# Kernel optimization log

Measured on AMD Instinct MI355X. Metric: run time of the kernel, lower is better.

## Reference

```python
import jax, jax.numpy as jnp
import numpy as np

NUM_HEADS = 8
HIDDEN = 8

def conv1x1(x, w):
    # x: [B,C,H,W], w: [O,C] -> [B,O,H,W]
    return jnp.einsum('oc,bchw->bohw', w, x)

def grid_sample_border(img, gx, gy):
    # Bilinear grid_sample, padding_mode='border', align_corners=True.
    # img: [B,C,H,W]; gx, gy: [B,H,W] normalized coords in [-1,1].
    B, C, H, W = img.shape
    ix = (gx + 1.0) * 0.5 * (W - 1)
    iy = (gy + 1.0) * 0.5 * (H - 1)
    x0f = jnp.floor(ix); y0f = jnp.floor(iy)
    wx = (ix - x0f)[..., None]; wy = (iy - y0f)[..., None]
    x0 = x0f.astype(jnp.int32); y0 = y0f.astype(jnp.int32)
    x0c = jnp.clip(x0, 0, W - 1); x1c = jnp.clip(x0 + 1, 0, W - 1)
    y0c = jnp.clip(y0, 0, H - 1); y1c = jnp.clip(y0 + 1, 0, H - 1)
    imt = jnp.transpose(img, (0, 2, 3, 1))  # [B,H,W,C]
    b = jnp.arange(B)[:, None, None]
    v00 = imt[b, y0c, x0c]; v01 = imt[b, y0c, x1c]
    v10 = imt[b, y1c, x0c]; v11 = imt[b, y1c, x1c]
    out = (v00 * (1 - wx) * (1 - wy) + v01 * wx * (1 - wy)
           + v10 * (1 - wx) * wy + v11 * wx * wy)
    return jnp.transpose(out, (0, 3, 1, 2))

def process_sub(cur, ref, Wq, Wk, Wv, Wver, Whor):
    B, C, H, W = cur.shape
    c = HIDDEN // NUM_HEADS  # per-head channel dim (=1)
    q = conv1x1(cur, Wq).reshape(B, NUM_HEADS, c, H, W)
    k = conv1x1(ref, Wk).reshape(B, NUM_HEADS, c, H, W)
    v = conv1x1(ref, Wv).reshape(B, NUM_HEADS, c, H, W)
    # vertical axial attention (each column w independent, attend over rows)
    a_ver = jax.nn.softmax(jnp.einsum('bkchw,bkclw->bkwhl', q, k), axis=-1)
    o_ver = jnp.einsum('bkwhl,bkclw->bkchw', a_ver, v).reshape(B, HIDDEN, H, W)
    o_ver = conv1x1(o_ver, Wver)[:, 0]  # [B,H,W]
    # horizontal axial attention (each row h independent, attend over cols)
    a_hor = jax.nn.softmax(jnp.einsum('bkchw,bkchl->bkhwl', q, k), axis=-1)
    o_hor = jnp.einsum('bkhwl,bkchl->bkchw', a_hor, v).reshape(B, HIDDEN, H, W)
    o_hor = conv1x1(o_hor, Whor)[:, 0]  # [B,H,W]
    # identity grid + flow
    ys = -1.0 + 2.0 * jnp.arange(H, dtype=cur.dtype) / max(float(H - 1), 1.0)
    xs = -1.0 + 2.0 * jnp.arange(W, dtype=cur.dtype) / max(float(W - 1), 1.0)
    gx = xs[None, None, :] + o_hor / ((W - 1.0) / 2.0)
    gy = ys[None, :, None] + o_ver / ((H - 1.0) / 2.0)
    return grid_sample_border(ref, gx, gy)

def _forward(cur_fea, ref_fea, Wq, Wk, Wv, Wver, Whor):
    B, C, H, W = cur_fea.shape
    def split(x):
        return jnp.stack([x[:, :, ::2, ::2], x[:, :, 1::2, 1::2],
                          x[:, :, ::2, 1::2], x[:, :, 1::2, ::2]], 0)
    cur_sub = split(cur_fea).reshape(4 * B, C, H // 2, W // 2)
    ref_sub = split(ref_fea).reshape(4 * B, C, H // 2, W // 2)
    warped = process_sub(cur_sub, ref_sub, Wq, Wk, Wv, Wver, Whor)
    ul, br, ur, bl = warped.reshape(4, B, C, H // 2, W // 2)
    out = jnp.zeros((B, C, H, W), dtype=jnp.float32)
    out = out.at[:, :, ::2, ::2].set(ul)
    out = out.at[:, :, ::2, 1::2].set(ur)
    out = out.at[:, :, 1::2, ::2].set(bl)
    out = out.at[:, :, 1::2, 1::2].set(br)
    return out

def setup_inputs() -> dict:
    key = jax.random.key(0)
    ks = jax.random.split(key, 7)
    B, C, H, W = 2, 64, 256, 256
    return {
        'cur_fea': jax.random.normal(ks[0], (B, C, H, W), jnp.float32),
        'ref_fea': jax.random.normal(ks[1], (B, C, H, W), jnp.float32),
        'Wq': jax.random.normal(ks[2], (HIDDEN, C), jnp.float32) * 0.05,
        'Wk': jax.random.normal(ks[3], (HIDDEN, C), jnp.float32) * 0.05,
        'Wv': jax.random.normal(ks[4], (HIDDEN, C), jnp.float32) * 0.05,
        'Wver': jax.random.normal(ks[5], (1, HIDDEN), jnp.float32) * 0.05,
        'Whor': jax.random.normal(ks[6], (1, HIDDEN), jnp.float32) * 0.05,
    }

def reference(cur_fea, ref_fea, Wq, Wk, Wv, Wver, Whor):
    return _forward(cur_fea, ref_fea, Wq, Wk, Wv, Wver, Whor)
```

## Files before the change

kernel.cpp:

```cpp
#include <hip/hip_runtime.h>


constexpr int PLANE = 16384;
constexpr float LOG2E = 1.4426950408889634f;

typedef float v2f __attribute__((ext_vector_type(2)));

static __device__ __forceinline__ v2f pk_mul(v2f a, v2f b) {
    v2f d;
    asm("v_pk_mul_f32 %0, %1, %2" : "=v"(d) : "v"(a), "v"(b));
    return d;
}
static __device__ __forceinline__ void pk_addi(v2f& d, v2f a) {
    asm("v_pk_add_f32 %0, %0, %1" : "+v"(d) : "v"(a));
}
static __device__ __forceinline__ void pk_fmai(v2f& d, v2f a, v2f b) {
    asm("v_pk_fma_f32 %0, %1, %2, %0" : "+v"(d) : "v"(a), "v"(b));
}

__global__ __launch_bounds__(64) void prep_w(
    const float* __restrict__ Wq, const float* __restrict__ Wk,
    const float* __restrict__ Wv, float* __restrict__ WTg)
{
    const int c = threadIdx.x;
#pragma unroll
    for (int j = 0; j < 8; ++j) {
        WTg[c * 24 + j]      = Wq[j * 64 + c];
        WTg[c * 24 + 8 + j]  = LOG2E * Wk[j * 64 + c];
        WTg[c * 24 + 16 + j] = Wv[j * 64 + c];
    }
}

__global__ __launch_bounds__(512) void qkv_kernel(
    const float* __restrict__ cur, const float* __restrict__ ref,
    const float* __restrict__ WTg,
    float* __restrict__ Q, float* __restrict__ K, float* __restrict__ V)
{
    __shared__ float red0[128 * 25];
    __shared__ float red1[128 * 25];
    const int tid = threadIdx.x;

    const int bi = blockIdx.x;
    const int b  = bi >> 9;
    const int Y  = (bi >> 1) & 255;
    const int Xh = bi & 1;
    const int cg = tid >> 7;
    const int xi = tid & 127;
    const int X  = Xh * 128 + xi;

    const size_t base_in = (size_t)b * 64 * 65536 + (size_t)Y * 256 + X;
    const float* curp = cur + base_in;
    const float* refp = ref + base_in;

    float q[8], k[8], v[8];
#pragma unroll
    for (int i = 0; i < 8; ++i) { q[i] = 0.f; k[i] = 0.f; v[i] = 0.f; }

    const int c0 = __builtin_amdgcn_readfirstlane(cg * 16);
#pragma unroll 8
    for (int c = 0; c < 16; ++c) {
        float cu = curp[(size_t)(c0 + c) * 65536];
        float rf = refp[(size_t)(c0 + c) * 65536];
        const float* wr = &WTg[(c0 + c) * 24];
#pragma unroll
        for (int i = 0; i < 8; ++i) {
            q[i] = fmaf(wr[i],      cu, q[i]);
            k[i] = fmaf(wr[8 + i],  rf, k[i]);
            v[i] = fmaf(wr[16 + i], rf, v[i]);
        }
    }

    float* row0 = &red0[xi * 25];
    float* row1 = &red1[xi * 25];
    if (cg == 1) {
#pragma unroll
        for (int i = 0; i < 8; ++i) {
            row0[i] = q[i]; row0[8 + i] = k[i]; row0[16 + i] = v[i];
        }
    } else if (cg == 3) {
#pragma unroll
        for (int i = 0; i < 8; ++i) {
            row1[i] = q[i]; row1[8 + i] = k[i]; row1[16 + i] = v[i];
        }
    }
    __syncthreads();
    if (cg == 2) {
#pragma unroll
        for (int i = 0; i < 8; ++i) {
            row1[i]      += q[i];
            row1[8 + i]  += k[i];
            row1[16 + i] += v[i];
        }
    } else if (cg == 0) {
#pragma unroll
        for (int i = 0; i < 8; ++i) {
            q[i] += row0[i]; k[i] += row0[8 + i]; v[i] += row0[16 + i];
        }
    }
    __syncthreads();
    if (cg == 0) {
        const int dy = Y & 1, dx = X & 1;
        const int p  = dy ? (dx ? 1 : 3) : (dx ? 2 : 0);
        const int sb = p * 2 + b;
        const int h = Y >> 1, w = X >> 1;
#pragma unroll
        for (int i = 0; i < 8; ++i) {
            const size_t o = ((size_t)(sb * 8 + i) << 14) + (h << 7) + w;
            Q[o] = q[i] + row1[i];
            K[o] = k[i] + row1[8 + i];
            V[o] = v[i] + row1[16 + i];
        }
    }
}

__global__ __launch_bounds__(256) void attn_fused(
    const float* __restrict__ Q, const float* __restrict__ K,
    const float* __restrict__ V,
    const float* __restrict__ Whor, const float* __restrict__ Wver,
    float* __restrict__ OH, float* __restrict__ OVT)
{
    __shared__ __align__(16) float kk[4][2 * 132];
    __shared__ __align__(16) float vv[4][2 * 132];
    __shared__ float part[4 * 128];

    const int pass = blockIdx.x >> 10;
    const int P    = blockIdx.x & 1023;
    int sb, line;
    if (!pass) {
        sb   = P >> 7;
        line = P & 127;
    } else {
        const int w4 = P & 7, wl = P >> 6;
        sb   = (P >> 3) & 7;
        line = (w4 << 4) | wl;
    }
    const float* __restrict__ wsel = pass ? Wver : Whor;
    float* __restrict__ o = pass ? OVT : OH;

    const int tid  = threadIdx.x;
    const int wv   = tid >> 6;
    const int lane = tid & 63;
    const size_t sbb = ((size_t)(sb * 8)) << 14;

    size_t qb0, qb1;
    if (!pass) {
        qb0 = sbb + ((size_t)line << 7) + lane;
        qb1 = qb0 + 64;
    } else {
        qb0 = sbb + ((size_t)lane << 7) + line;
        qb1 = qb0 + ((size_t)64 << 7);
    }

    float qv00, qv01, qv10, qv11;
    {
        const int h0 = 2 * wv, h1 = 2 * wv + 1;
        qv00 = Q[qb0 + ((size_t)h0 << 14)];
        qv01 = Q[qb1 + ((size_t)h0 << 14)];
        qv10 = Q[qb0 + ((size_t)h1 << 14)];
        qv11 = Q[qb1 + ((size_t)h1 << 14)];
    }

    {
        const int hl = lane >> 5;
        const int hh = 2 * wv + hl;
        const int fi = lane & 31;
        float* kd = &kk[wv][hl * 132 + (fi << 2)];
        float* vd = &vv[wv][hl * 132 + (fi << 2)];
        if (!pass) {
            const size_t g = sbb + ((size_t)hh << 14) + ((size_t)line << 7) + (fi << 2);
            *(float4*)kd = *(const float4*)&K[g];
            *(float4*)vd = *(const float4*)&V[g];
        } else {
            const size_t g = sbb + ((size_t)hh << 14) + ((size_t)(fi << 2) << 7) + line;
            float4 kq, vq;
            kq.x = K[g];       kq.y = K[g + 128];
            kq.z = K[g + 256]; kq.w = K[g + 384];
            vq.x = V[g];       vq.y = V[g + 128];
            vq.z = V[g + 256]; vq.w = V[g + 384];
            *(float4*)kd = kq;
            *(float4*)vd = vq;
        }
    }
    asm volatile("s_waitcnt lgkmcnt(0)" ::: "memory");

    float acc0 = 0.f, acc1 = 0.f;
#pragma unroll
    for (int i = 0; i < 2; ++i) {
        const int head = 2 * wv + i;
        const float q0 = i ? qv10 : qv00;
        const float q1 = i ? qv11 : qv01;
        const v2f s0 = { q0, q0 };
        const v2f s1 = { q1, q1 };
        const float4* k4 = (const float4*)&kk[wv][i * 132];
        const float4* v4 = (const float4*)&vv[wv][i * 132];
        v2f dA0 = {0.f, 0.f}, dB0 = {0.f, 0.f};
        v2f nA0 = {0.f, 0.f}, nB0 = {0.f, 0.f};
        v2f dA1 = {0.f, 0.f}, dB1 = {0.f, 0.f};
        v2f nA1 = {0.f, 0.f}, nB1 = {0.f, 0.f};
#pragma unroll 8
        for (int l = 0; l < 32; ++l) {
            const float4 kq = k4[l];
            const float4 vq = v4[l];
            const v2f k01 = { kq.x, kq.y }, k23 = { kq.z, kq.w };
            const v2f v01 = { vq.x, vq.y }, v23 = { vq.z, vq.w };
            const v2f a0 = pk_mul(s0, k01);
            const v2f b0 = pk_mul(s0, k23);
            const v2f e0 = { __builtin_amdgcn_exp2f(a0.x), __builtin_amdgcn_exp2f(a0.y) };
            const v2f f0 = { __builtin_amdgcn_exp2f(b0.x), __builtin_amdgcn_exp2f(b0.y) };
            pk_addi(dA0, e0);
            pk_addi(dB0, f0);
            pk_fmai(nA0, e0, v01);
            pk_fmai(nB0, f0, v23);
            const v2f a1 = pk_mul(s1, k01);
            const v2f b1 = pk_mul(s1, k23);
            const v2f e1 = { __builtin_amdgcn_exp2f(a1.x), __builtin_amdgcn_exp2f(a1.y) };
            const v2f f1 = { __builtin_amdgcn_exp2f(b1.x), __builtin_amdgcn_exp2f(b1.y) };
            pk_addi(dA1, e1);
            pk_addi(dB1, f1);
            pk_fmai(nA1, e1, v01);
            pk_fmai(nB1, f1, v23);
        }
        const float wh = wsel[head];
        pk_addi(dA0, dB0); pk_addi(nA0, nB0);
        pk_addi(dA1, dB1); pk_addi(nA1, nB1);
        acc0 = fmaf(wh, (nA0.x + nA0.y) * __builtin_amdgcn_rcpf(dA0.x + dA0.y), acc0);
        acc1 = fmaf(wh, (nA1.x + nA1.y) * __builtin_amdgcn_rcpf(dA1.x + dA1.y), acc1);
    }

    part[wv * 128 + lane]      = acc0;
    part[wv * 128 + lane + 64] = acc1;
    __syncthreads();
    if (tid < 128) {
        const float s = (part[tid] + part[256 + tid])
                      + (part[128 + tid] + part[384 + tid]);
        o[((size_t)sb << 14) + ((size_t)line << 7) + tid] = s;
    }
}

__global__ __launch_bounds__(256) void warp_kernel(
    const float* __restrict__ ref, const float* __restrict__ ovt,
    const float* __restrict__ oh, float* __restrict__ out)
{
    const int bi = blockIdx.x;
    const int Y  = bi & 255;
    const int cg = (bi >> 8) & 3;
    const int b  = bi >> 10;
    const int X  = threadIdx.x;

    const int dy = Y & 1, dx = X & 1;
    const int p  = dy ? (dx ? 1 : 3) : (dx ? 2 : 0);
    const int sb = p * 2 + b;
    const int h = Y >> 1, w = X >> 1;

    const float ix = (float)w + oh [((size_t)sb << 14) + (h << 7) + w];
    const float iy = (float)h + ovt[((size_t)sb << 14) + (w << 7) + h];

    const float x0f = floorf(ix), y0f = floorf(iy);
    const float wx = ix - x0f,    wy = iy - y0f;
    const int x0 = (int)x0f, y0 = (int)y0f;
    const int x0c = min(max(x0, 0), 127),     x1c = min(max(x0 + 1, 0), 127);
    const int y0c = min(max(y0, 0), 127),     y1c = min(max(y0 + 1, 0), 127);

    const float w00 = (1.f - wx) * (1.f - wy);
    const float w01 = wx * (1.f - wy);
    const float w10 = (1.f - wx) * wy;
    const float w11 = wx * wy;

    const int cb  = min(2 * x0c, 252);
    const bool hi  = (x0c == 127);
    const bool up1 = hi | (x1c != x0c);
    const int r0 = (2 * y0c + dy) * 256, r1 = (2 * y1c + dy) * 256;
    const int dst = Y * 256 + X;

    const float* rp = ref + ((size_t)b * 64 + cg * 16) * 65536;
    float* op = out + ((size_t)b * 64 + cg * 16) * 65536;

#pragma unroll 4
    for (int c = 0; c < 16; ++c) {
        const size_t pl = (size_t)c * 65536;
        const float4 f0 = *(const float4*)&rp[pl + r0 + cb];
        const float4 f1 = *(const float4*)&rp[pl + r1 + cb];
        const float L0 = dx ? f0.y : f0.x, H0 = dx ? f0.w : f0.z;
        const float L1 = dx ? f1.y : f1.x, H1 = dx ? f1.w : f1.z;
        const float v00 = hi ? H0 : L0,  v01 = up1 ? H0 : L0;
        const float v10 = hi ? H1 : L1,  v11 = up1 ? H1 : L1;
        op[pl + dst] = fmaf(w00, v00, fmaf(w01, v01, fmaf(w10, v10, w11 * v11)));
    }
}

extern "C" void kernel_launch(void* const* d_in, const int* in_sizes, int n_in,
                              void* d_out, int out_size, void* d_ws, size_t ws_size,
                              hipStream_t stream)
{
    const float* cur  = (const float*)d_in[0];
    const float* ref  = (const float*)d_in[1];
    const float* Wq   = (const float*)d_in[2];
    const float* Wk   = (const float*)d_in[3];
    const float* Wv   = (const float*)d_in[4];
    const float* Wver = (const float*)d_in[5];
    const float* Whor = (const float*)d_in[6];
    float* out = (float*)d_out;

    float* ws = (float*)d_ws;
    const size_t NQ = 8 * 8 * (size_t)PLANE;
    float* Q   = ws;
    float* K   = Q  + NQ;
    float* V   = K  + NQ;
    float* OVT = V  + NQ;
    float* OH  = OVT + 8 * (size_t)PLANE;
    float* WTg = OH  + 8 * (size_t)PLANE;

    prep_w<<<1, 64, 0, stream>>>(Wq, Wk, Wv, WTg);
    qkv_kernel<<<1024, 512, 0, stream>>>(cur, ref, WTg, Q, K, V);
    attn_fused<<<2048, 256, 0, stream>>>(Q, K, V, Whor, Wver, OH, OVT);
    warp_kernel<<<2048, 256, 0, stream>>>(ref, OVT, OH, out);
}
```

Baseline: 166.6 us.

## Fuse horizontal axial attention into the QKV projection kernel

The QKV projection kernel now processes a full image row per 1024-thread block and keeps the projected q/k/v for that row in shared memory. It then runs the horizontal attention for both sub-image parities directly from shared memory and writes OH. This removes the separate horizontal attention pass and its reload of Q/K/V from global memory. The cost is a larger block with heavy shared memory use (about 33 KB) and extra barriers, which may limit occupancy. The vertical pass remains a separate kernel.

```diff
diff --git a/kernel.cpp b/kernel.cpp
--- a/kernel.cpp
+++ b/kernel.cpp
@@ -31,24 +31,24 @@
     }
 }
 
-__global__ __launch_bounds__(512) void qkv_kernel(
+__global__ __launch_bounds__(1024, 8) void qkv_attnh(
     const float* __restrict__ cur, const float* __restrict__ ref,
-    const float* __restrict__ WTg,
-    float* __restrict__ Q, float* __restrict__ K, float* __restrict__ V)
-{
-    __shared__ float red0[128 * 25];
-    __shared__ float red1[128 * 25];
+    const float* __restrict__ WTg, const float* __restrict__ Whor,
+    float* __restrict__ Q, float* __restrict__ K, float* __restrict__ V,
+    float* __restrict__ OH)
+{
+    __shared__ __align__(16) float smem0[256 * 25];
+    __shared__ float red1[256 * 25];
+    __shared__ float part[2 * 8 * 128];
+
     const int tid = threadIdx.x;
-
-    const int bi = blockIdx.x;
-    const int b  = bi >> 9;
-    const int Y  = (bi >> 1) & 255;
-    const int Xh = bi & 1;
-    const int cg = tid >> 7;
-    const int xi = tid & 127;
-    const int X  = Xh * 128 + xi;
-
-    const size_t base_in = (size_t)b * 64 * 65536 + (size_t)Y * 256 + X;
+    const int bi  = blockIdx.x;
+    const int b   = bi >> 8;
+    const int Y   = bi & 255;
+    const int cg  = tid >> 8;
+    const int xi  = tid & 255;
+
+    const size_t base_in = (size_t)b * 64 * 65536 + (size_t)Y * 256 + xi;
     const float* curp = cur + base_in;
     const float* refp = ref + base_in;
 
@@ -70,7 +70,7 @@
         }
     }
 
-    float* row0 = &red0[xi * 25];
+    float* row0 = &smem0[xi * 25];
     float* row1 = &red1[xi * 25];
     if (cg == 1) {
 #pragma unroll
@@ -98,58 +98,116 @@
         }
     }
     __syncthreads();
+
+    float* qq = smem0 + 4224;
+    float* kk = smem0;
+    float* vv = smem0 + 2112;
+
+    const int dy = Y & 1;
     if (cg == 0) {
-        const int dy = Y & 1, dx = X & 1;
+        const int dx = xi & 1;
         const int p  = dy ? (dx ? 1 : 3) : (dx ? 2 : 0);
         const int sb = p * 2 + b;
-        const int h = Y >> 1, w = X >> 1;
-#pragma unroll
-        for (int i = 0; i < 8; ++i) {
+        const int h = Y >> 1, w = xi >> 1;
+#pragma unroll
+        for (int i = 0; i < 8; ++i) {
+            const float qf = q[i] + row1[i];
+            const float kf = k[i] + row1[8 + i];
+            const float vf = v[i] + row1[16 + i];
             const size_t o = ((size_t)(sb * 8 + i) << 14) + (h << 7) + w;
-            Q[o] = q[i] + row1[i];
-            K[o] = k[i] + row1[8 + i];
-            V[o] = v[i] + row1[16 + i];
-        }
-    }
-}
-
-__global__ __launch_bounds__(256) void attn_fused(
+            Q[o] = qf; K[o] = kf; V[o] = vf;
+            qq[(dx * 8 + i) * 128 + w] = qf;
+            kk[(dx * 8 + i) * 132 + w] = kf;
+            vv[(dx * 8 + i) * 132 + w] = vf;
+        }
+    }
+    __syncthreads();
+
+    {
+        const int wv16 = tid >> 6;
+        const int lane = tid & 63;
+        const int head = wv16 & 7;
+        const int dxw  = wv16 >> 3;
+        const int hrow = dxw * 8 + head;
+        const float q0 = qq[hrow * 128 + lane];
+        const float q1 = qq[hrow * 128 + lane + 64];
+        const v2f s0 = { q0, q0 };
+        const v2f s1 = { q1, q1 };
+        const float4* k4 = (const float4*)&kk[hrow * 132];
+        const float4* v4 = (const float4*)&vv[hrow * 132];
+        v2f dA0 = {0.f, 0.f}, dB0 = {0.f, 0.f};
+        v2f nA0 = {0.f, 0.f}, nB0 = {0.f, 0.f};
+        v2f dA1 = {0.f, 0.f}, dB1 = {0.f, 0.f};
+        v2f nA1 = {0.f, 0.f}, nB1 = {0.f, 0.f};
+#pragma unroll 8
+        for (int l = 0; l < 32; ++l) {
+            const float4 kq = k4[l];
+            const float4 vq = v4[l];
+            const v2f k01 = { kq.x, kq.y }, k23 = { kq.z, kq.w };
+            const v2f v01 = { vq.x, vq.y }, v23 = { vq.z, vq.w };
+            const v2f a0 = pk_mul(s0, k01);
+            const v2f b0 = pk_mul(s0, k23);
+            const v2f e0 = { __builtin_amdgcn_exp2f(a0.x), __builtin_amdgcn_exp2f(a0.y) };
+            const v2f f0 = { __builtin_amdgcn_exp2f(b0.x), __builtin_amdgcn_exp2f(b0.y) };
+            pk_addi(dA0, e0);
+            pk_addi(dB0, f0);
+            pk_fmai(nA0, e0, v01);
+            pk_fmai(nB0, f0, v23);
+            const v2f a1 = pk_mul(s1, k01);
+            const v2f b1 = pk_mul(s1, k23);
+            const v2f e1 = { __builtin_amdgcn_exp2f(a1.x), __builtin_amdgcn_exp2f(a1.y) };
+            const v2f f1 = { __builtin_amdgcn_exp2f(b1.x), __builtin_amdgcn_exp2f(b1.y) };
+            pk_addi(dA1, e1);
+            pk_addi(dB1, f1);
+            pk_fmai(nA1, e1, v01);
+            pk_fmai(nB1, f1, v23);
+        }
+        const float wh = Whor[head];
+        pk_addi(dA0, dB0); pk_addi(nA0, nB0);
+        pk_addi(dA1, dB1); pk_addi(nA1, nB1);
+        part[hrow * 128 + lane] =
+            wh * ((nA0.x + nA0.y) * __builtin_amdgcn_rcpf(dA0.x + dA0.y));
+        part[hrow * 128 + lane + 64] =
+            wh * ((nA1.x + nA1.y) * __builtin_amdgcn_rcpf(dA1.x + dA1.y));
+    }
+    __syncthreads();
+
+    if (tid < 256) {
+        const int dxw = tid >> 7;
+        const int w   = tid & 127;
+        const int base = dxw * 8 * 128 + w;
+        const float s =
+            (((part[base]       + part[base + 128]) +
+              (part[base + 256] + part[base + 384])) +
+             ((part[base + 512] + part[base + 640]) +
+              (part[base + 768] + part[base + 896])));
+        const int p  = dy ? (dxw ? 1 : 3) : (dxw ? 2 : 0);
+        const int sb = p * 2 + b;
+        OH[((size_t)sb << 14) + ((size_t)(Y >> 1) << 7) + w] = s;
+    }
+}
+
+__global__ __launch_bounds__(256) void attn_v(
     const float* __restrict__ Q, const float* __restrict__ K,
     const float* __restrict__ V,
-    const float* __restrict__ Whor, const float* __restrict__ Wver,
-    float* __restrict__ OH, float* __restrict__ OVT)
+    const float* __restrict__ Wver, float* __restrict__ OVT)
 {
     __shared__ __align__(16) float kk[4][2 * 132];
     __shared__ __align__(16) float vv[4][2 * 132];
     __shared__ float part[4 * 128];
 
-    const int pass = blockIdx.x >> 10;
-    const int P    = blockIdx.x & 1023;
-    int sb, line;
-    if (!pass) {
-        sb   = P >> 7;
-        line = P & 127;
-    } else {
-        const int w4 = P & 7, wl = P >> 6;
-        sb   = (P >> 3) & 7;
-        line = (w4 << 4) | wl;
-    }
-    const float* __restrict__ wsel = pass ? Wver : Whor;
-    float* __restrict__ o = pass ? OVT : OH;
+    const int P  = blockIdx.x;
+    const int w4 = P & 7, wl = P >> 6;
+    const int sb   = (P >> 3) & 7;
+    const int line = (w4 << 4) | wl;
 
     const int tid  = threadIdx.x;
     const int wv   = tid >> 6;
     const int lane = tid & 63;
     const size_t sbb = ((size_t)(sb * 8)) << 14;
 
-    size_t qb0, qb1;
-    if (!pass) {
-        qb0 = sbb + ((size_t)line << 7) + lane;
-        qb1 = qb0 + 64;
-    } else {
-        qb0 = sbb + ((size_t)lane << 7) + line;
-        qb1 = qb0 + ((size_t)64 << 7);
-    }
+    const size_t qb0 = sbb + ((size_t)lane << 7) + line;
+    const size_t qb1 = qb0 + ((size_t)64 << 7);
 
     float qv00, qv01, qv10, qv11;
     {
@@ -164,22 +222,14 @@
         const int hl = lane >> 5;
         const int hh = 2 * wv + hl;
         const int fi = lane & 31;
-        float* kd = &kk[wv][hl * 132 + (fi << 2)];
-        float* vd = &vv[wv][hl * 132 + (fi << 2)];
-        if (!pass) {
-            const size_t g = sbb + ((size_t)hh << 14) + ((size_t)line << 7) + (fi << 2);
-            *(float4*)kd = *(const float4*)&K[g];
-            *(float4*)vd = *(const float4*)&V[g];
-        } else {
-            const size_t g = sbb + ((size_t)hh << 14) + ((size_t)(fi << 2) << 7) + line;
-            float4 kq, vq;
-            kq.x = K[g];       kq.y = K[g + 128];
-            kq.z = K[g + 256]; kq.w = K[g + 384];
-            vq.x = V[g];       vq.y = V[g + 128];
-            vq.z = V[g + 256]; vq.w = V[g + 384];
-            *(float4*)kd = kq;
-            *(float4*)vd = vq;
-        }
+        const size_t g = sbb + ((size_t)hh << 14) + ((size_t)(fi << 2) << 7) + line;
+        float4 kq, vq;
+        kq.x = K[g];       kq.y = K[g + 128];
+        kq.z = K[g + 256]; kq.w = K[g + 384];
+        vq.x = V[g];       vq.y = V[g + 128];
+        vq.z = V[g + 256]; vq.w = V[g + 384];
+        *(float4*)&kk[wv][hl * 132 + (fi << 2)] = kq;
+        *(float4*)&vv[wv][hl * 132 + (fi << 2)] = vq;
     }
     asm volatile("s_waitcnt lgkmcnt(0)" ::: "memory");
 
@@ -220,7 +270,7 @@
             pk_fmai(nA1, e1, v01);
             pk_fmai(nB1, f1, v23);
         }
-        const float wh = wsel[head];
+        const float wh = Wver[head];
         pk_addi(dA0, dB0); pk_addi(nA0, nB0);
         pk_addi(dA1, dB1); pk_addi(nA1, nB1);
         acc0 = fmaf(wh, (nA0.x + nA0.y) * __builtin_amdgcn_rcpf(dA0.x + dA0.y), acc0);
@@ -233,7 +283,7 @@
     if (tid < 128) {
         const float s = (part[tid] + part[256 + tid])
                       + (part[128 + tid] + part[384 + tid]);
-        o[((size_t)sb << 14) + ((size_t)line << 7) + tid] = s;
+        OVT[((size_t)sb << 14) + ((size_t)line << 7) + tid] = s;
     }
 }
 
@@ -311,7 +361,7 @@
     float* WTg = OH  + 8 * (size_t)PLANE;
 
     prep_w<<<1, 64, 0, stream>>>(Wq, Wk, Wv, WTg);
-    qkv_kernel<<<1024, 512, 0, stream>>>(cur, ref, WTg, Q, K, V);
-    attn_fused<<<2048, 256, 0, stream>>>(Q, K, V, Whor, Wver, OH, OVT);
+    qkv_attnh<<<512, 1024, 0, stream>>>(cur, ref, WTg, Whor, Q, K, V, OH);
+    attn_v<<<1024, 256, 0, stream>>>(Q, K, V, Wver, OVT);
     warp_kernel<<<2048, 256, 0, stream>>>(ref, OVT, OH, out);
 }
```

Measured after the change: 178.4 us. 1.07x slower.
